# Kernel tuning notes

Hardware: AMD Instinct MI355X
Metric: run time of the kernel (lower is better)

Reference implementation:

```python
import jax, jax.numpy as jnp
import numpy as np

B, NF, FD = 2048, 64, 32   # batch, n_features, feature_dim
S = NF // 2                # n_sites
D, OD = 32, 32             # bond_dim, out_dim


def setup_inputs() -> dict:
    key = jax.random.key(0)
    k1, k2, k3, k4 = jax.random.split(key, 4)
    sc = 1.0 / np.sqrt(FD * D)
    x = jax.random.normal(k1, (B, NF, FD), dtype=jnp.float32)
    L = jax.random.normal(k2, (S, FD, D, D), dtype=jnp.float32) * sc
    R = jax.random.normal(k3, (S, FD, D, D), dtype=jnp.float32) * sc
    O = jax.random.normal(k4, (S, D, D, OD), dtype=jnp.float32) * sc
    bias = jnp.zeros((S, OD), dtype=jnp.float32)
    return {"x": x, "L": L, "R": R, "O": O, "bias": bias}


def reference(x, L, R, O, bias):
    # x: [B, 2*S, FD] -> left/right features per site
    xL = x[:, 0::2, :]  # [B, S, FD]
    xR = x[:, 1::2, :]  # [B, S, FD]
    # feature -> bond matrices
    A = jnp.einsum('bsf,sfam->bsam', xL, L)   # [B, S, D, D]
    Bm = jnp.einsum('bsg,sgan->bsan', xR, R)  # [B, S, D, D]
    # contract shared bond leg a, then output tensor
    M = jnp.einsum('bsam,bsan->bsmn', A, Bm)  # [B, S, D, D]
    out = jnp.einsum('bsmn,smno->bso', M, O)  # [B, S, OD]
    return out + bias  # bias broadcast over batch; activation is None
```

## Files before the change

kernel.cpp:

```cpp
#include <hip/hip_runtime.h>
#include <hip/hip_bf16.h>

typedef __attribute__((ext_vector_type(4)))  _Float16 h4;
typedef __attribute__((ext_vector_type(8)))  _Float16 h8;
typedef __attribute__((ext_vector_type(4)))  float f32x4;
typedef __attribute__((ext_vector_type(16))) float f32x16;

__global__ __launch_bounds__(64) void conv_kernel(
    const float* __restrict__ Rg, const float* __restrict__ Og,
    _Float16* __restrict__ Rb, char* __restrict__ Opp)
{
    __shared__ float tile[32][33];
    const int bid = blockIdx.x;
    const int s = bid & 31, q = (bid >> 5) & 31, which = bid >> 10;
    const int t = threadIdx.x, tl = t & 31, th = t >> 5;

    if (which == 0) {
        #pragma unroll
        for (int j = 0; j < 16; ++j) {
            int ar = 2*j + th;
            tile[tl][ar] = Rg[(((size_t)s*32 + q)*32 + ar)*32 + tl];
        }
        __syncthreads();
        _Float16* dst = Rb + ((size_t)s*32 + q)*1024;
        #pragma unroll
        for (int it = 0; it < 4; ++it) {
            int nr = it*8 + (t >> 3), a0 = (t & 7)*4;
            h4 w;
            #pragma unroll
            for (int k = 0; k < 4; ++k) w[k] = (_Float16)tile[nr][a0 + k];
            *(h4*)(dst + nr*32 + a0) = w;
        }
    } else {
        #pragma unroll
        for (int j = 0; j < 16; ++j) {
            int nr = 2*j + th;
            tile[tl][nr] = Og[(((size_t)s*32 + q)*32 + nr)*32 + tl];
        }
        __syncthreads();
        char* dst = Opp + (size_t)s*65536 + q*2048;
        int o = t & 31, cq = t >> 5;
        #pragma unroll
        for (int it = 0; it < 2; ++it) {
            int c = it*2 + cq;
            h8 w;
            #pragma unroll
            for (int k = 0; k < 8; ++k) w[k] = (_Float16)tile[o][c*8 + k];
            *(h8*)(dst + c*512 + o*16) = w;
        }
    }
}

__global__ __launch_bounds__(256, 2) void tmake_kernel(
    const float* __restrict__ Lg, const _Float16* __restrict__ Rb,
    const char* __restrict__ Opp, char* __restrict__ Tp)
{
    __shared__ __align__(16) char Wl[65536];
    const int bid = blockIdx.x;
    const int s = bid & 31, f = bid >> 5;
    const int t = threadIdx.x, wid = t >> 6, l = t & 63;
    const int llo = l & 15, lhi = l >> 4;

    const float* Lsf = Lg + ((size_t)s*32 + f)*1024;
    h8 bfr[2];
    #pragma unroll
    for (int mt = 0; mt < 2; ++mt)
        #pragma unroll
        for (int j = 0; j < 8; ++j)
            bfr[mt][j] = (_Float16)Lsf[(8*lhi + j)*32 + mt*16 + llo];

    const _Float16* Rbs = Rb + (size_t)s*32768;

    #pragma unroll 4
    for (int nt = 0; nt < 16; ++nt) {
        int gnb = (wid*16 + nt)*16;
        h8 af = *(const h8*)(Rbs + (gnb + llo)*32 + 8*lhi);
        int g = gnb >> 5;
        int nbase = (gnb & 31) + 4*lhi;
        #pragma unroll
        for (int mt = 0; mt < 2; ++mt) {
            f32x4 d = __builtin_amdgcn_mfma_f32_16x16x32_f16(af, bfr[mt], (f32x4)(0.f), 0, 0, 0);
            int m = mt*16 + llo;
            h4 w;
            #pragma unroll
            for (int r = 0; r < 4; ++r) w[r] = (_Float16)d[r];
            int byte = (g*2048 + m*64 + nbase*2) ^ ((((g & 7) ^ (m & 7))) << 4);
            *(h4*)(Wl + byte) = w;
        }
    }
    __syncthreads();

    const int ot = wid & 1, kq = wid >> 1;
    const int orow = ot*16 + llo;
    const char* Opps = Opp + (size_t)s*65536;
    f32x4 acc0 = (f32x4)(0.f), acc1 = (f32x4)(0.f);
    #pragma unroll 4
    for (int ksl = 0; ksl < 16; ++ksl) {
        int ks = kq*16 + ksl;
        h8 bf = *(const h8*)(Opps + (ks*4 + lhi)*512 + orow*16);
        {
            int grow = llo;
            int byte = (grow*2048 + ks*64 + lhi*16) ^ ((((grow & 7) ^ (ks & 7))) << 4);
            h8 af = *(const h8*)(Wl + byte);
            acc0 = __builtin_amdgcn_mfma_f32_16x16x32_f16(af, bf, acc0, 0, 0, 0);
        }
        {
            int grow = 16 + llo;
            int byte = (grow*2048 + ks*64 + lhi*16) ^ ((((grow & 7) ^ (ks & 7))) << 4);
            h8 af = *(const h8*)(Wl + byte);
            acc1 = __builtin_amdgcn_mfma_f32_16x16x32_f16(af, bf, acc1, 0, 0, 0);
        }
    }
    __syncthreads();
    if (kq == 1) {
        *(f32x4*)(Wl + ((ot*2 + 0)*64 + l)*16) = acc0;
        *(f32x4*)(Wl + ((ot*2 + 1)*64 + l)*16) = acc1;
    }
    __syncthreads();
    if (kq == 0) {
        acc0 += *(const f32x4*)(Wl + ((ot*2 + 0)*64 + l)*16);
        acc1 += *(const f32x4*)(Wl + ((ot*2 + 1)*64 + l)*16);
        char* Tps = Tp + (size_t)s*65536;
        h4 w0, w1;
        #pragma unroll
        for (int r = 0; r < 4; ++r) { w0[r] = (_Float16)acc0[r]; w1[r] = (_Float16)acc1[r]; }
        *(h4*)(Tps + (f*2 + 0)*1024 + orow*32 + lhi*8) = w0;
        *(h4*)(Tps + (f*2 + 1)*1024 + orow*32 + lhi*8) = w1;
    }
}

__global__ __launch_bounds__(256, 3) void main_kernel(
    const float* __restrict__ x, const char* __restrict__ Tp,
    const float* __restrict__ bias, float* __restrict__ out)
{
    __shared__ __align__(16) char Tb0[16384];
    __shared__ __align__(16) char Tb1[16384];
    __shared__ __align__(16) char xl2[8192];
    __shared__ __align__(16) char xr2[8192];

    const int bid = blockIdx.x;
    const int s = bid & 31;
    const int b0 = (bid >> 5) * 128;
    const int t = threadIdx.x, wid = t >> 6, l = t & 63;
    const int lo5 = l & 31, hi = l >> 5;
    const int kh = wid & 1, sbp = wid >> 1;

    const char* Tps = Tp + (size_t)s*65536;

    uint4 tv[4];
    #pragma unroll
    for (int i = 0; i < 4; ++i)
        tv[i] = *(const uint4*)(Tps + (i*256 + t)*16);

    #pragma unroll
    for (int i = 0; i < 8; ++i) {
        int idx = i*256 + t, b = idx >> 4, c = idx & 15;
        float4 v = *(const float4*)(x + (size_t)(b0 + b)*2048 + s*64 + c*4);
        h4 w; w[0] = (_Float16)v.x; w[1] = (_Float16)v.y;
              w[2] = (_Float16)v.z; w[3] = (_Float16)v.w;
        if (c < 8) *(h4*)(xl2 + (c >> 1)*2048 + b*16 + (c & 1)*8) = w;
        else { int c2 = c - 8; *(h4*)(xr2 + (c2 >> 1)*2048 + b*16 + (c2 & 1)*8) = w; }
    }
    #pragma unroll
    for (int i = 0; i < 4; ++i)
        *(uint4*)(Tb0 + (i*256 + t)*16) = tv[i];
    #pragma unroll
    for (int i = 0; i < 4; ++i)
        tv[i] = *(const uint4*)(Tps + 16384 + (i*256 + t)*16);
    __syncthreads();

    h4 xlh[2][4];
    h8 xrh[2][2];
    #pragma unroll
    for (int sb = 0; sb < 2; ++sb) {
        int b = sbp*64 + sb*32 + lo5;
        #pragma unroll
        for (int c = 0; c < 4; ++c)
            xlh[sb][c] = *(const h4*)(xl2 + c*2048 + b*16 + kh*8);
        #pragma unroll
        for (int gh = 0; gh < 2; ++gh)
            xrh[sb][gh] = *(const h8*)(xr2 + (gh*2 + hi)*2048 + b*16);
    }

    f32x16 acc0 = (f32x16)(0.f), acc1 = (f32x16)(0.f);

    #pragma unroll
    for (int c = 0; c < 4; ++c) {
        const char* Tc = (c & 1) ? Tb1 : Tb0;
        #pragma unroll
        for (int i = 0; i < 8; ++i) {
            int ksl = kh*8 + i;
            h8 bf = *(const h8*)(Tc + ksl*1024 + lo5*32 + hi*16);
            _Float16 x0 = xlh[0][c][i >> 1];
            _Float16 x1 = xlh[1][c][i >> 1];
            h8 z0 = xrh[0][i & 1] * x0;
            acc0 = __builtin_amdgcn_mfma_f32_32x32x16_f16(z0, bf, acc0, 0, 0, 0);
            h8 z1 = xrh[1][i & 1] * x1;
            acc1 = __builtin_amdgcn_mfma_f32_32x32x16_f16(z1, bf, acc1, 0, 0, 0);
        }
        if (c < 3) {
            char* Tn = (c & 1) ? Tb0 : Tb1;
            #pragma unroll
            for (int i = 0; i < 4; ++i)
                *(uint4*)(Tn + (i*256 + t)*16) = tv[i];
            if (c < 2) {
                #pragma unroll
                for (int i = 0; i < 4; ++i)
                    tv[i] = *(const uint4*)(Tps + (c + 2)*16384 + (i*256 + t)*16);
            }
            __syncthreads();
        }
    }

    __syncthreads();
    if (kh == 1) {
        #pragma unroll
        for (int rq = 0; rq < 4; ++rq) {
            f32x4 p0, p1;
            #pragma unroll
            for (int rr = 0; rr < 4; ++rr) { p0[rr] = acc0[rq*4 + rr]; p1[rr] = acc1[rq*4 + rr]; }
            *(f32x4*)(xl2 + sbp*4096 + rq*1024 + l*16) = p0;
            *(f32x4*)(xr2 + sbp*4096 + rq*1024 + l*16) = p1;
        }
    }
    __syncthreads();
    if (kh == 0) {
        const float bv = bias[s*32 + lo5];
        #pragma unroll
        for (int rq = 0; rq < 4; ++rq) {
            f32x4 p0 = *(const f32x4*)(xl2 + sbp*4096 + rq*1024 + l*16);
            f32x4 p1 = *(const f32x4*)(xr2 + sbp*4096 + rq*1024 + l*16);
            #pragma unroll
            for (int rr = 0; rr < 4; ++rr) {
                int r = rq*4 + rr;
                int rowoff = (r & 3) + 8*(r >> 2) + 4*hi;
                out[(size_t)(b0 + sbp*64 + rowoff)*1024 + s*32 + lo5] = acc0[r] + p0[rr] + bv;
                out[(size_t)(b0 + sbp*64 + 32 + rowoff)*1024 + s*32 + lo5] = acc1[r] + p1[rr] + bv;
            }
        }
    }
}

extern "C" void kernel_launch(void* const* d_in, const int* in_sizes, int n_in,
                              void* d_out, int out_size, void* d_ws, size_t ws_size,
                              hipStream_t stream) {
    const float* x    = (const float*)d_in[0];
    const float* L    = (const float*)d_in[1];
    const float* R    = (const float*)d_in[2];
    const float* O    = (const float*)d_in[3];
    const float* bias = (const float*)d_in[4];
    float* out = (float*)d_out;

    _Float16* Rb  = (_Float16*)d_ws;
    char*     Opp = (char*)(Rb + 1048576);
    char*     Tp  = Opp + 2097152;

    conv_kernel<<<dim3(2048), 64, 0, stream>>>(R, O, Rb, Opp);
    tmake_kernel<<<dim3(1024), 256, 0, stream>>>(L, Rb, Opp, Tp);
    main_kernel<<<dim3(512), 256, 0, stream>>>(x, Tp, bias, out);
}
```

Measured before the change: 33.99 us.

## Halve batch tile per block, double grid, and coalesce output via LDS staging

```diff
diff --git a/kernel.cpp b/kernel.cpp
--- a/kernel.cpp
+++ b/kernel.cpp
@@ -129,18 +129,17 @@
     }
 }
 
-__global__ __launch_bounds__(256, 3) void main_kernel(
+__global__ __launch_bounds__(256, 4) void main_kernel(
     const float* __restrict__ x, const char* __restrict__ Tp,
     const float* __restrict__ bias, float* __restrict__ out)
 {
     __shared__ __align__(16) char Tb0[16384];
     __shared__ __align__(16) char Tb1[16384];
-    __shared__ __align__(16) char xl2[8192];
-    __shared__ __align__(16) char xr2[8192];
+    __shared__ __align__(16) char xbuf[8192];
 
     const int bid = blockIdx.x;
-    const int s = bid & 31;
-    const int b0 = (bid >> 5) * 128;
+    const int btile = bid & 31, s = bid >> 5;
+    const int b0 = btile * 64;
     const int t = threadIdx.x, wid = t >> 6, l = t & 63;
     const int lo5 = l & 31, hi = l >> 5;
     const int kh = wid & 1, sbp = wid >> 1;
@@ -152,37 +151,42 @@
     for (int i = 0; i < 4; ++i)
         tv[i] = *(const uint4*)(Tps + (i*256 + t)*16);
 
-    #pragma unroll
-    for (int i = 0; i < 8; ++i) {
+    float4 xv[4];
+    #pragma unroll
+    for (int i = 0; i < 4; ++i) {
         int idx = i*256 + t, b = idx >> 4, c = idx & 15;
-        float4 v = *(const float4*)(x + (size_t)(b0 + b)*2048 + s*64 + c*4);
+        xv[i] = *(const float4*)(x + (size_t)(b0 + b)*2048 + s*64 + c*4);
+    }
+
+    #pragma unroll
+    for (int i = 0; i < 4; ++i)
+        *(uint4*)(Tb0 + (i*256 + t)*16) = tv[i];
+    #pragma unroll
+    for (int i = 0; i < 4; ++i)
+        tv[i] = *(const uint4*)(Tps + 16384 + (i*256 + t)*16);
+
+    #pragma unroll
+    for (int i = 0; i < 4; ++i) {
+        int idx = i*256 + t, b = idx >> 4, c = idx & 15;
+        float4 v = xv[i];
         h4 w; w[0] = (_Float16)v.x; w[1] = (_Float16)v.y;
               w[2] = (_Float16)v.z; w[3] = (_Float16)v.w;
-        if (c < 8) *(h4*)(xl2 + (c >> 1)*2048 + b*16 + (c & 1)*8) = w;
-        else { int c2 = c - 8; *(h4*)(xr2 + (c2 >> 1)*2048 + b*16 + (c2 & 1)*8) = w; }
-    }
-    #pragma unroll
-    for (int i = 0; i < 4; ++i)
-        *(uint4*)(Tb0 + (i*256 + t)*16) = tv[i];
-    #pragma unroll
-    for (int i = 0; i < 4; ++i)
-        tv[i] = *(const uint4*)(Tps + 16384 + (i*256 + t)*16);
-    __syncthreads();
-
-    h4 xlh[2][4];
-    h8 xrh[2][2];
-    #pragma unroll
-    for (int sb = 0; sb < 2; ++sb) {
-        int b = sbp*64 + sb*32 + lo5;
-        #pragma unroll
-        for (int c = 0; c < 4; ++c)
-            xlh[sb][c] = *(const h4*)(xl2 + c*2048 + b*16 + kh*8);
-        #pragma unroll
-        for (int gh = 0; gh < 2; ++gh)
-            xrh[sb][gh] = *(const h8*)(xr2 + (gh*2 + hi)*2048 + b*16);
-    }
-
-    f32x16 acc0 = (f32x16)(0.f), acc1 = (f32x16)(0.f);
+        if (c < 8) *(h4*)(xbuf + (c >> 1)*1024 + b*16 + (c & 1)*8) = w;
+        else { int c2 = c - 8; *(h4*)(xbuf + 4096 + (c2 >> 1)*1024 + b*16 + (c2 & 1)*8) = w; }
+    }
+    __syncthreads();
+
+    const int b = sbp*32 + lo5;
+    h4 xlh[4];
+    #pragma unroll
+    for (int c = 0; c < 4; ++c)
+        xlh[c] = *(const h4*)(xbuf + c*1024 + b*16 + kh*8);
+    h8 xrh[2];
+    #pragma unroll
+    for (int gh = 0; gh < 2; ++gh)
+        xrh[gh] = *(const h8*)(xbuf + 4096 + (gh*2 + hi)*1024 + b*16);
+
+    f32x16 acc_e = (f32x16)(0.f), acc_o = (f32x16)(0.f);
 
     #pragma unroll
     for (int c = 0; c < 4; ++c) {
@@ -191,12 +195,10 @@
         for (int i = 0; i < 8; ++i) {
             int ksl = kh*8 + i;
             h8 bf = *(const h8*)(Tc + ksl*1024 + lo5*32 + hi*16);
-            _Float16 x0 = xlh[0][c][i >> 1];
-            _Float16 x1 = xlh[1][c][i >> 1];
-            h8 z0 = xrh[0][i & 1] * x0;
-            acc0 = __builtin_amdgcn_mfma_f32_32x32x16_f16(z0, bf, acc0, 0, 0, 0);
-            h8 z1 = xrh[1][i & 1] * x1;
-            acc1 = __builtin_amdgcn_mfma_f32_32x32x16_f16(z1, bf, acc1, 0, 0, 0);
+            _Float16 xs = xlh[c][i >> 1];
+            h8 z = xrh[i & 1] * xs;
+            if (i & 1) acc_o = __builtin_amdgcn_mfma_f32_32x32x16_f16(z, bf, acc_o, 0, 0, 0);
+            else       acc_e = __builtin_amdgcn_mfma_f32_32x32x16_f16(z, bf, acc_e, 0, 0, 0);
         }
         if (c < 3) {
             char* Tn = (c & 1) ? Tb0 : Tb1;
@@ -212,32 +214,25 @@
         }
     }
 
-    __syncthreads();
-    if (kh == 1) {
-        #pragma unroll
-        for (int rq = 0; rq < 4; ++rq) {
-            f32x4 p0, p1;
-            #pragma unroll
-            for (int rr = 0; rr < 4; ++rr) { p0[rr] = acc0[rq*4 + rr]; p1[rr] = acc1[rq*4 + rr]; }
-            *(f32x4*)(xl2 + sbp*4096 + rq*1024 + l*16) = p0;
-            *(f32x4*)(xr2 + sbp*4096 + rq*1024 + l*16) = p1;
-        }
-    }
-    __syncthreads();
-    if (kh == 0) {
-        const float bv = bias[s*32 + lo5];
-        #pragma unroll
-        for (int rq = 0; rq < 4; ++rq) {
-            f32x4 p0 = *(const f32x4*)(xl2 + sbp*4096 + rq*1024 + l*16);
-            f32x4 p1 = *(const f32x4*)(xr2 + sbp*4096 + rq*1024 + l*16);
-            #pragma unroll
-            for (int rr = 0; rr < 4; ++rr) {
-                int r = rq*4 + rr;
-                int rowoff = (r & 3) + 8*(r >> 2) + 4*hi;
-                out[(size_t)(b0 + sbp*64 + rowoff)*1024 + s*32 + lo5] = acc0[r] + p0[rr] + bv;
-                out[(size_t)(b0 + sbp*64 + 32 + rowoff)*1024 + s*32 + lo5] = acc1[r] + p1[rr] + bv;
-            }
-        }
+    f32x16 acc = acc_e + acc_o;
+
+    #pragma unroll
+    for (int r = 0; r < 16; ++r) {
+        int row = sbp*32 + (r & 3) + 8*(r >> 2) + 4*hi;
+        *(float*)(Tb0 + kh*8192 + row*128 + lo5*4) = acc[r];
+    }
+    __syncthreads();
+
+    const float* bias_s = bias + s*32;
+    #pragma unroll
+    for (int k = 0; k < 2; ++k) {
+        int u = k*256 + t;
+        int row = u >> 3, colq = u & 7;
+        f32x4 v0 = *(const f32x4*)(Tb0 + u*16);
+        f32x4 v1 = *(const f32x4*)(Tb0 + 8192 + u*16);
+        f32x4 bv = *(const f32x4*)(bias_s + colq*4);
+        f32x4 res = v0 + v1 + bv;
+        *(f32x4*)(out + (size_t)(b0 + row)*1024 + s*32 + colq*4) = res;
     }
 }
 
@@ -252,10 +247,10 @@
     float* out = (float*)d_out;
 
     _Float16* Rb  = (_Float16*)d_ws;
-    char*     Opp = (char*)(Rb + 1048576);
-    char*     Tp  = Opp + 2097152;
+    char*     Opp = (char*)d_ws + 2097152;
+    char*     Tp  = (char*)d_ws + 4194304;
 
     conv_kernel<<<dim3(2048), 64, 0, stream>>>(R, O, Rb, Opp);
     tmake_kernel<<<dim3(1024), 256, 0, stream>>>(L, Rb, Opp, Tp);
-    main_kernel<<<dim3(512), 256, 0, stream>>>(x, Tp, bias, out);
-}
+    main_kernel<<<dim3(1024), 256, 0, stream>>>(x, Tp, bias, out);
+}
```

After: 39.17 us. 1.15x slower.
